# Kernel optimization log

Hardware: AMD Instinct MI355X
Metric: run time of the kernel (lower is better)

The kernel has to match this reference:

```python
import jax, jax.numpy as jnp
import numpy as np

R_MAX = 1.0
BASIS_MASK = 0xFF        # low 8 bits -> basis index (basis_size=256)
R_BITS_MASK = 0xFFFF     # next 16 bits -> quantized radius
R_DENOM = 65535.0
INT8_DENOM = 127.0


def setup_inputs() -> dict:
    key = jax.random.key(0)
    k_x, k_c, k_b, k_r, k_s, k_bias = jax.random.split(key, 6)
    B, S, D_in, D_out, BASIS = 4, 2048, 4096, 4096, 256
    x = jax.random.normal(k_x, (B, S, D_in), dtype=jnp.float32)
    codes = jax.random.randint(k_c, (D_out,), 0, 16777216, dtype=jnp.int32)
    basis_table = jax.random.normal(k_b, (BASIS, D_in), dtype=jnp.float32)
    residual_q = jax.random.randint(k_r, (D_out, D_in), 0, 256, dtype=jnp.int32)
    residual_scales = jax.random.uniform(k_s, (D_out,), dtype=jnp.float32) * 0.05
    bias = jax.random.normal(k_bias, (D_out,), dtype=jnp.float32)
    return {"x": x, "codes": codes, "basis_table": basis_table,
            "residual_q": residual_q, "residual_scales": residual_scales,
            "bias": bias}


def decode_weight(codes, basis_table, residual_q, residual_scales):
    # Bitfield decode: low 8 bits = basis index, next 16 bits = quantized radius in [0, r_max].
    idx = codes & BASIS_MASK                                   # [O]
    r = ((codes >> 8) & R_BITS_MASK).astype(jnp.float32) / R_DENOM * R_MAX  # [O]
    base = r[:, None] * basis_table[idx]                       # [O, I]
    resid = (residual_q.astype(jnp.float32) - 128.0) / INT8_DENOM  # dequant int8 residual
    return base + residual_scales[:, None] * resid             # [O, I]


def reference(x, codes, basis_table, residual_q, residual_scales, bias):
    W = decode_weight(codes, basis_table, residual_q, residual_scales)  # [O, I]
    # y = x @ W^T + bias  (fused dequant-matmul in the original CUDA kernel)
    return jnp.einsum("bsi,oi->bso", x, W) + bias
```

## Files before the change

### kernel.cpp

```cpp
#include <hip/hip_runtime.h>


typedef __bf16 bf16x8 __attribute__((ext_vector_type(8)));
typedef float f32x4 __attribute__((ext_vector_type(4)));
typedef unsigned short u16x8 __attribute__((ext_vector_type(8)));

__device__ __forceinline__ unsigned short f2bf(float f) {
    union { float f; unsigned int u; } c; c.f = f;
    unsigned int u = c.u;
    u += 0x7fffu + ((u >> 16) & 1u);
    return (unsigned short)(u >> 16);
}

__device__ __forceinline__ void load_lds16(const void* g, void* l) {
    __builtin_amdgcn_global_load_lds(
        (__attribute__((address_space(1))) void*)(void*)g,
        (__attribute__((address_space(3))) void*)l,
        16, 0, 0);
}

__global__ void decode_w_kernel(const int* __restrict__ codes,
                                const float* __restrict__ basis,
                                const int* __restrict__ q,
                                const float* __restrict__ scales,
                                unsigned short* __restrict__ Wb, int K) {
    const int o = blockIdx.x;
    const int code = codes[o];
    const int bi = code & 0xFF;
    const float r = (float)((code >> 8) & 0xFFFF) * (1.0f / 65535.0f);
    const float s = scales[o];
    const float* brow = basis + (size_t)bi * K;
    const int*   qrow = q     + (size_t)o  * K;
    unsigned short* wrow = Wb + (size_t)o  * K;
    const float inv127 = 1.0f / 127.0f;
    for (int i = threadIdx.x * 4; i < K; i += blockDim.x * 4) {
        float4 b4 = *(const float4*)(brow + i);
        int4   q4 = *(const int4*)(qrow + i);
        ushort4 w;
        w.x = f2bf(r * b4.x + s * (float)(q4.x - 128) * inv127);
        w.y = f2bf(r * b4.y + s * (float)(q4.y - 128) * inv127);
        w.z = f2bf(r * b4.z + s * (float)(q4.z - 128) * inv127);
        w.w = f2bf(r * b4.w + s * (float)(q4.w - 128) * inv127);
        *(ushort4*)(wrow + i) = w;
    }
}

__global__ void cvt_x_kernel(const float4* __restrict__ x4,
                             ushort4* __restrict__ xb4, int n4) {
    int i = blockIdx.x * blockDim.x + threadIdx.x;
    const int stride = gridDim.x * blockDim.x;
    for (; i < n4; i += stride) {
        float4 v = x4[i];
        ushort4 o;
        o.x = f2bf(v.x); o.y = f2bf(v.y); o.z = f2bf(v.z); o.w = f2bf(v.w);
        xb4[i] = o;
    }
}

#define TILE_M 128
#define TILE_N 128
#define TILE_K 32

__global__ void gemm_bt_kernel(const unsigned short* __restrict__ Xb,
                               const unsigned short* __restrict__ Wb,
                               const float* __restrict__ bias,
                               float* __restrict__ out,
                               int M, int N, int K) {
    __shared__ __align__(16) unsigned short As[TILE_M * TILE_K];
    __shared__ __align__(16) unsigned short Bs[TILE_N * TILE_K];

    const int tid  = threadIdx.x;
    const int lane = tid & 63;
    const int wv   = tid >> 6;
    const int wrow = wv >> 1;
    const int wcol = wv & 1;
    const int m0 = blockIdx.y * TILE_M;
    const int n0 = blockIdx.x * TILE_N;

    const int lr = lane & 15;
    const int kg = lane >> 4;

    f32x4 acc[4][4];
#pragma unroll
    for (int mi = 0; mi < 4; ++mi)
#pragma unroll
        for (int ni = 0; ni < 4; ++ni)
            acc[mi][ni] = (f32x4){0.f, 0.f, 0.f, 0.f};

    const int lin0 = tid, lin1 = tid + 256;
    const int ar0 = lin0 >> 2, ac0 = (lin0 & 3) * 8;
    const int ar1 = lin1 >> 2, ac1 = (lin1 & 3) * 8;

    const unsigned short* Ag0 = Xb + (size_t)(m0 + ar0) * K + ac0;
    const unsigned short* Ag1 = Xb + (size_t)(m0 + ar1) * K + ac1;
    const unsigned short* Bg0 = Wb + (size_t)(n0 + ar0) * K + ac0;
    const unsigned short* Bg1 = Wb + (size_t)(n0 + ar1) * K + ac1;

    unsigned short* Al0 = As + lin0 * 8;
    unsigned short* Al1 = As + lin1 * 8;
    unsigned short* Bl0 = Bs + lin0 * 8;
    unsigned short* Bl1 = Bs + lin1 * 8;

    for (int k0 = 0; k0 < K; k0 += TILE_K) {
        load_lds16(Ag0 + k0, Al0);
        load_lds16(Ag1 + k0, Al1);
        load_lds16(Bg0 + k0, Bl0);
        load_lds16(Bg1 + k0, Bl1);
        __syncthreads();

        bf16x8 af[4], bfr[4];
#pragma unroll
        for (int mi = 0; mi < 4; ++mi) {
            u16x8 raw = *(const u16x8*)(As + (wrow * 64 + mi * 16 + lr) * TILE_K + kg * 8);
            af[mi] = __builtin_bit_cast(bf16x8, raw);
        }
#pragma unroll
        for (int ni = 0; ni < 4; ++ni) {
            u16x8 raw = *(const u16x8*)(Bs + (wcol * 64 + ni * 16 + lr) * TILE_K + kg * 8);
            bfr[ni] = __builtin_bit_cast(bf16x8, raw);
        }
#pragma unroll
        for (int mi = 0; mi < 4; ++mi)
#pragma unroll
            for (int ni = 0; ni < 4; ++ni)
                acc[mi][ni] = __builtin_amdgcn_mfma_f32_16x16x32_bf16(
                    af[mi], bfr[ni], acc[mi][ni], 0, 0, 0);
        __syncthreads();
    }

#pragma unroll
    for (int ni = 0; ni < 4; ++ni) {
        const int n = n0 + wcol * 64 + ni * 16 + lr;
        const float bv = bias[n];
#pragma unroll
        for (int mi = 0; mi < 4; ++mi) {
            const int mbase = m0 + wrow * 64 + mi * 16 + kg * 4;
#pragma unroll
            for (int rg = 0; rg < 4; ++rg)
                out[(size_t)(mbase + rg) * N + n] = acc[mi][ni][rg] + bv;
        }
    }
}

extern "C" void kernel_launch(void* const* d_in, const int* in_sizes, int n_in,
                              void* d_out, int out_size, void* d_ws, size_t ws_size,
                              hipStream_t stream) {
    const float* x        = (const float*)d_in[0];
    const int*   codes    = (const int*)d_in[1];
    const float* basis    = (const float*)d_in[2];
    const int*   q        = (const int*)d_in[3];
    const float* scales   = (const float*)d_in[4];
    const float* bias     = (const float*)d_in[5];
    float* out = (float*)d_out;

    const int BASIS = 256;
    const int K = in_sizes[2] / BASIS;
    const int N = in_sizes[1];
    const int M = in_sizes[0] / K;

    unsigned short* Xb = (unsigned short*)d_ws;
    unsigned short* Wb = Xb + (size_t)M * K;

    const int n4 = (M * K) / 4;
    cvt_x_kernel<<<4096, 256, 0, stream>>>((const float4*)x, (ushort4*)Xb, n4);

    decode_w_kernel<<<N, 256, 0, stream>>>(codes, basis, q, scales, Wb, K);

    dim3 grid(N / TILE_N, M / TILE_M);
    gemm_bt_kernel<<<grid, 256, 0, stream>>>(Xb, Wb, bias, out, M, N, K);
}
```

Measured before the change: 568.9 us.

## Split weight into basis projection plus int8 residual GEMM with quantized activations

Rewrites y = x·W^T as r·(x·basis^T)[c] plus a residual term. The basis term becomes a small M×256 bf16 GEMM; the residual term becomes an int8 MFMA GEMM over per-row quantized activations and packed int8 residuals. The scales, gathered basis product and bias are applied in the epilogue. This removes materializing the dequantized weight and doubles MFMA throughput per instruction, at the cost of int8 activation quantization error and an extra gather from P in the epilogue.

```diff
diff --git a/kernel.cpp b/kernel.cpp
--- a/kernel.cpp
+++ b/kernel.cpp
@@ -3,14 +3,8 @@
 
 typedef __bf16 bf16x8 __attribute__((ext_vector_type(8)));
 typedef float f32x4 __attribute__((ext_vector_type(4)));
+typedef int i32x4 __attribute__((ext_vector_type(4)));
 typedef unsigned short u16x8 __attribute__((ext_vector_type(8)));
-
-__device__ __forceinline__ unsigned short f2bf(float f) {
-    union { float f; unsigned int u; } c; c.f = f;
-    unsigned int u = c.u;
-    u += 0x7fffu + ((u >> 16) & 1u);
-    return (unsigned short)(u >> 16);
-}
 
 __device__ __forceinline__ void load_lds16(const void* g, void* l) {
     __builtin_amdgcn_global_load_lds(
@@ -19,125 +13,236 @@
         16, 0, 0);
 }
 
-__global__ void decode_w_kernel(const int* __restrict__ codes,
-                                const float* __restrict__ basis,
-                                const int* __restrict__ q,
-                                const float* __restrict__ scales,
-                                unsigned short* __restrict__ Wb, int K) {
-    const int o = blockIdx.x;
-    const int code = codes[o];
-    const int bi = code & 0xFF;
-    const float r = (float)((code >> 8) & 0xFFFF) * (1.0f / 65535.0f);
-    const float s = scales[o];
-    const float* brow = basis + (size_t)bi * K;
-    const int*   qrow = q     + (size_t)o  * K;
-    unsigned short* wrow = Wb + (size_t)o  * K;
-    const float inv127 = 1.0f / 127.0f;
-    for (int i = threadIdx.x * 4; i < K; i += blockDim.x * 4) {
-        float4 b4 = *(const float4*)(brow + i);
-        int4   q4 = *(const int4*)(qrow + i);
-        ushort4 w;
-        w.x = f2bf(r * b4.x + s * (float)(q4.x - 128) * inv127);
-        w.y = f2bf(r * b4.y + s * (float)(q4.y - 128) * inv127);
-        w.z = f2bf(r * b4.z + s * (float)(q4.z - 128) * inv127);
-        w.w = f2bf(r * b4.w + s * (float)(q4.w - 128) * inv127);
-        *(ushort4*)(wrow + i) = w;
-    }
-}
-
-__global__ void cvt_x_kernel(const float4* __restrict__ x4,
-                             ushort4* __restrict__ xb4, int n4) {
-    int i = blockIdx.x * blockDim.x + threadIdx.x;
-    const int stride = gridDim.x * blockDim.x;
-    for (; i < n4; i += stride) {
-        float4 v = x4[i];
-        ushort4 o;
-        o.x = f2bf(v.x); o.y = f2bf(v.y); o.z = f2bf(v.z); o.w = f2bf(v.w);
-        xb4[i] = o;
-    }
-}
-
-#define TILE_M 128
-#define TILE_N 128
-#define TILE_K 32
-
-__global__ void gemm_bt_kernel(const unsigned short* __restrict__ Xb,
-                               const unsigned short* __restrict__ Wb,
+__global__ void quant_x_kernel(const float* __restrict__ x,
+                               signed char* __restrict__ xq,
+                               float* __restrict__ arow, int K) {
+    const int m = blockIdx.x;
+    const float* row = x + (size_t)m * K;
+    const int base = threadIdx.x * 16;
+    float4 v[4];
+#pragma unroll
+    for (int j = 0; j < 4; ++j) v[j] = *(const float4*)(row + base + j * 4);
+
+    float lmax = 0.f;
+#pragma unroll
+    for (int j = 0; j < 4; ++j) {
+        lmax = fmaxf(lmax, fabsf(v[j].x));
+        lmax = fmaxf(lmax, fabsf(v[j].y));
+        lmax = fmaxf(lmax, fabsf(v[j].z));
+        lmax = fmaxf(lmax, fabsf(v[j].w));
+    }
+#pragma unroll
+    for (int off = 32; off; off >>= 1)
+        lmax = fmaxf(lmax, __shfl_xor(lmax, off));
+    __shared__ float smax[4];
+    if ((threadIdx.x & 63) == 0) smax[threadIdx.x >> 6] = lmax;
+    __syncthreads();
+    const float mx = fmaxf(fmaxf(smax[0], smax[1]), fmaxf(smax[2], smax[3]));
+    const float inv = mx > 0.f ? 127.0f / mx : 0.0f;
+    if (threadIdx.x == 0) arow[m] = mx * (1.0f / 127.0f);
+
+    union { signed char c[16]; i32x4 w; } pk;
+#pragma unroll
+    for (int j = 0; j < 4; ++j) {
+        pk.c[j * 4 + 0] = (signed char)(int)rintf(v[j].x * inv);
+        pk.c[j * 4 + 1] = (signed char)(int)rintf(v[j].y * inv);
+        pk.c[j * 4 + 2] = (signed char)(int)rintf(v[j].z * inv);
+        pk.c[j * 4 + 3] = (signed char)(int)rintf(v[j].w * inv);
+    }
+    *(i32x4*)(xq + (size_t)m * K + base) = pk.w;
+}
+
+__global__ void pack_q_kernel(const int4* __restrict__ q4,
+                              unsigned int* __restrict__ out, int n4) {
+    const int i = blockIdx.x * blockDim.x + threadIdx.x;
+    if (i >= n4) return;
+    int4 a = q4[i];
+    unsigned int w = ((unsigned)(a.x - 128) & 0xFFu)
+                   | (((unsigned)(a.y - 128) & 0xFFu) << 8)
+                   | (((unsigned)(a.z - 128) & 0xFFu) << 16)
+                   | (((unsigned)(a.w - 128) & 0xFFu) << 24);
+    out[i] = w;
+}
+
+__global__ void p_gemm_kernel(const float* __restrict__ x,
+                              const float* __restrict__ basis,
+                              float* __restrict__ P,
+                              int M, int K) {
+    const int NB = 256;
+    __shared__ __align__(16) unsigned short As[64 * 32];
+    __shared__ __align__(16) unsigned short Bs[128 * 32];
+
+    const int tid  = threadIdx.x;
+    const int lane = tid & 63;
+    const int wv   = tid >> 6;
+    const int m0 = blockIdx.y * 64;
+    const int n0 = blockIdx.x * 128;
+    const int lr = lane & 15;
+    const int kg = lane >> 4;
+
+    f32x4 acc[4][2];
+#pragma unroll
+    for (int mi = 0; mi < 4; ++mi)
+#pragma unroll
+        for (int ni = 0; ni < 2; ++ni)
+            acc[mi][ni] = (f32x4){0.f, 0.f, 0.f, 0.f};
+
+    const int arow_ = tid >> 2, acol = (tid & 3) * 8;
+    const int lb0 = tid, lb1 = tid + 256;
+    const int br0 = lb0 >> 2, bc0 = (lb0 & 3) * 8;
+    const int br1 = lb1 >> 2, bc1 = (lb1 & 3) * 8;
+
+    const float* Agp = x + (size_t)(m0 + arow_) * K + acol;
+    const float* Bg0 = basis + (size_t)(n0 + br0) * K + bc0;
+    const float* Bg1 = basis + (size_t)(n0 + br1) * K + bc1;
+
+    for (int k0 = 0; k0 < K; k0 += 32) {
+        float4 a0 = *(const float4*)(Agp + k0);
+        float4 a1 = *(const float4*)(Agp + k0 + 4);
+        float4 b00 = *(const float4*)(Bg0 + k0);
+        float4 b01 = *(const float4*)(Bg0 + k0 + 4);
+        float4 b10 = *(const float4*)(Bg1 + k0);
+        float4 b11 = *(const float4*)(Bg1 + k0 + 4);
+        union { bf16x8 b; u16x8 u; } ca, cb0, cb1;
+        ca.b[0] = (__bf16)a0.x; ca.b[1] = (__bf16)a0.y;
+        ca.b[2] = (__bf16)a0.z; ca.b[3] = (__bf16)a0.w;
+        ca.b[4] = (__bf16)a1.x; ca.b[5] = (__bf16)a1.y;
+        ca.b[6] = (__bf16)a1.z; ca.b[7] = (__bf16)a1.w;
+        cb0.b[0] = (__bf16)b00.x; cb0.b[1] = (__bf16)b00.y;
+        cb0.b[2] = (__bf16)b00.z; cb0.b[3] = (__bf16)b00.w;
+        cb0.b[4] = (__bf16)b01.x; cb0.b[5] = (__bf16)b01.y;
+        cb0.b[6] = (__bf16)b01.z; cb0.b[7] = (__bf16)b01.w;
+        cb1.b[0] = (__bf16)b10.x; cb1.b[1] = (__bf16)b10.y;
+        cb1.b[2] = (__bf16)b10.z; cb1.b[3] = (__bf16)b10.w;
+        cb1.b[4] = (__bf16)b11.x; cb1.b[5] = (__bf16)b11.y;
+        cb1.b[6] = (__bf16)b11.z; cb1.b[7] = (__bf16)b11.w;
+        *(u16x8*)(As + tid * 8) = ca.u;
+        *(u16x8*)(Bs + lb0 * 8) = cb0.u;
+        *(u16x8*)(Bs + lb1 * 8) = cb1.u;
+        __syncthreads();
+
+        bf16x8 af[4], bfr[2];
+#pragma unroll
+        for (int mi = 0; mi < 4; ++mi)
+            af[mi] = __builtin_bit_cast(bf16x8,
+                *(const u16x8*)(As + (mi * 16 + lr) * 32 + kg * 8));
+#pragma unroll
+        for (int ni = 0; ni < 2; ++ni)
+            bfr[ni] = __builtin_bit_cast(bf16x8,
+                *(const u16x8*)(Bs + (wv * 32 + ni * 16 + lr) * 32 + kg * 8));
+#pragma unroll
+        for (int mi = 0; mi < 4; ++mi)
+#pragma unroll
+            for (int ni = 0; ni < 2; ++ni)
+                acc[mi][ni] = __builtin_amdgcn_mfma_f32_16x16x32_bf16(
+                    af[mi], bfr[ni], acc[mi][ni], 0, 0, 0);
+        __syncthreads();
+    }
+
+#pragma unroll
+    for (int ni = 0; ni < 2; ++ni) {
+        const int n = n0 + wv * 32 + ni * 16 + lr;
+#pragma unroll
+        for (int mi = 0; mi < 4; ++mi) {
+            const int mbase = m0 + mi * 16 + kg * 4;
+#pragma unroll
+            for (int rg = 0; rg < 4; ++rg)
+                P[(size_t)(mbase + rg) * NB + n] = acc[mi][ni][rg];
+        }
+    }
+}
+
+__global__ void gemm_i8_kernel(const signed char* __restrict__ Xq,
+                               const signed char* __restrict__ Qb,
+                               const float* __restrict__ arow,
+                               const int* __restrict__ codes,
+                               const float* __restrict__ scales,
                                const float* __restrict__ bias,
+                               const float* __restrict__ P,
                                float* __restrict__ out,
                                int M, int N, int K) {
-    __shared__ __align__(16) unsigned short As[TILE_M * TILE_K];
-    __shared__ __align__(16) unsigned short Bs[TILE_N * TILE_K];
+    __shared__ __align__(16) signed char As[128 * 64];
+    __shared__ __align__(16) signed char Bs[128 * 64];
 
     const int tid  = threadIdx.x;
     const int lane = tid & 63;
     const int wv   = tid >> 6;
     const int wrow = wv >> 1;
     const int wcol = wv & 1;
-    const int m0 = blockIdx.y * TILE_M;
-    const int n0 = blockIdx.x * TILE_N;
-
+    const int m0 = blockIdx.y * 128;
+    const int n0 = blockIdx.x * 128;
     const int lr = lane & 15;
     const int kg = lane >> 4;
 
-    f32x4 acc[4][4];
+    i32x4 acc[4][4];
 #pragma unroll
     for (int mi = 0; mi < 4; ++mi)
 #pragma unroll
         for (int ni = 0; ni < 4; ++ni)
-            acc[mi][ni] = (f32x4){0.f, 0.f, 0.f, 0.f};
+            acc[mi][ni] = (i32x4){0, 0, 0, 0};
 
     const int lin0 = tid, lin1 = tid + 256;
-    const int ar0 = lin0 >> 2, ac0 = (lin0 & 3) * 8;
-    const int ar1 = lin1 >> 2, ac1 = (lin1 & 3) * 8;
-
-    const unsigned short* Ag0 = Xb + (size_t)(m0 + ar0) * K + ac0;
-    const unsigned short* Ag1 = Xb + (size_t)(m0 + ar1) * K + ac1;
-    const unsigned short* Bg0 = Wb + (size_t)(n0 + ar0) * K + ac0;
-    const unsigned short* Bg1 = Wb + (size_t)(n0 + ar1) * K + ac1;
-
-    unsigned short* Al0 = As + lin0 * 8;
-    unsigned short* Al1 = As + lin1 * 8;
-    unsigned short* Bl0 = Bs + lin0 * 8;
-    unsigned short* Bl1 = Bs + lin1 * 8;
-
-    for (int k0 = 0; k0 < K; k0 += TILE_K) {
+    const int ar0 = lin0 >> 2, ac0 = (lin0 & 3) * 16;
+    const int ar1 = lin1 >> 2, ac1 = (lin1 & 3) * 16;
+
+    const signed char* Ag0 = Xq + (size_t)(m0 + ar0) * K + ac0;
+    const signed char* Ag1 = Xq + (size_t)(m0 + ar1) * K + ac1;
+    const signed char* Bg0 = Qb + (size_t)(n0 + ar0) * K + ac0;
+    const signed char* Bg1 = Qb + (size_t)(n0 + ar1) * K + ac1;
+
+    signed char* Al0 = As + lin0 * 16;
+    signed char* Al1 = As + lin1 * 16;
+    signed char* Bl0 = Bs + lin0 * 16;
+    signed char* Bl1 = Bs + lin1 * 16;
+
+    for (int k0 = 0; k0 < K; k0 += 64) {
         load_lds16(Ag0 + k0, Al0);
         load_lds16(Ag1 + k0, Al1);
         load_lds16(Bg0 + k0, Bl0);
         load_lds16(Bg1 + k0, Bl1);
         __syncthreads();
 
-        bf16x8 af[4], bfr[4];
-#pragma unroll
-        for (int mi = 0; mi < 4; ++mi) {
-            u16x8 raw = *(const u16x8*)(As + (wrow * 64 + mi * 16 + lr) * TILE_K + kg * 8);
-            af[mi] = __builtin_bit_cast(bf16x8, raw);
-        }
-#pragma unroll
-        for (int ni = 0; ni < 4; ++ni) {
-            u16x8 raw = *(const u16x8*)(Bs + (wcol * 64 + ni * 16 + lr) * TILE_K + kg * 8);
-            bfr[ni] = __builtin_bit_cast(bf16x8, raw);
-        }
+        i32x4 af[4], bfr[4];
+#pragma unroll
+        for (int mi = 0; mi < 4; ++mi)
+            af[mi] = *(const i32x4*)(As + (wrow * 64 + mi * 16 + lr) * 64 + kg * 16);
+#pragma unroll
+        for (int ni = 0; ni < 4; ++ni)
+            bfr[ni] = *(const i32x4*)(Bs + (wcol * 64 + ni * 16 + lr) * 64 + kg * 16);
 #pragma unroll
         for (int mi = 0; mi < 4; ++mi)
 #pragma unroll
             for (int ni = 0; ni < 4; ++ni)
-                acc[mi][ni] = __builtin_amdgcn_mfma_f32_16x16x32_bf16(
+                acc[mi][ni] = __builtin_amdgcn_mfma_i32_16x16x64_i8(
                     af[mi], bfr[ni], acc[mi][ni], 0, 0, 0);
         __syncthreads();
     }
+
+    float av[4][4];
+#pragma unroll
+    for (int mi = 0; mi < 4; ++mi)
+#pragma unroll
+        for (int rg = 0; rg < 4; ++rg)
+            av[mi][rg] = arow[m0 + wrow * 64 + mi * 16 + kg * 4 + rg];
 
 #pragma unroll
     for (int ni = 0; ni < 4; ++ni) {
         const int n = n0 + wcol * 64 + ni * 16 + lr;
+        const int code = codes[n];
+        const int c = code & 0xFF;
+        const float r = (float)((code >> 8) & 0xFFFF) * (1.0f / 65535.0f);
+        const float so = scales[n] * (1.0f / 127.0f);
         const float bv = bias[n];
 #pragma unroll
         for (int mi = 0; mi < 4; ++mi) {
             const int mbase = m0 + wrow * 64 + mi * 16 + kg * 4;
 #pragma unroll
-            for (int rg = 0; rg < 4; ++rg)
-                out[(size_t)(mbase + rg) * N + n] = acc[mi][ni][rg] + bv;
+            for (int rg = 0; rg < 4; ++rg) {
+                const int m = mbase + rg;
+                const float y = av[mi][rg] * so * (float)acc[mi][ni][rg]
+                              + r * P[(size_t)m * 256 + c] + bv;
+                out[(size_t)m * N + n] = y;
+            }
         }
     }
 }
@@ -158,14 +263,19 @@
     const int N = in_sizes[1];
     const int M = in_sizes[0] / K;
 
-    unsigned short* Xb = (unsigned short*)d_ws;
-    unsigned short* Wb = Xb + (size_t)M * K;
-
-    const int n4 = (M * K) / 4;
-    cvt_x_kernel<<<4096, 256, 0, stream>>>((const float4*)x, (ushort4*)Xb, n4);
-
-    decode_w_kernel<<<N, 256, 0, stream>>>(codes, basis, q, scales, Wb, K);
-
-    dim3 grid(N / TILE_N, M / TILE_M);
-    gemm_bt_kernel<<<grid, 256, 0, stream>>>(Xb, Wb, bias, out, M, N, K);
-}
+    char* ws = (char*)d_ws;
+    signed char* Xq = (signed char*)ws;
+    size_t off = (size_t)M * K;
+    float* Arow = (float*)(ws + off);
+    off += (size_t)M * sizeof(float);
+    signed char* Qb = (signed char*)(ws + off);
+    off += (size_t)N * K;
+    float* P = (float*)(ws + off);
+
+    quant_x_kernel<<<M, 256, 0, stream>>>(x, Xq, Arow, K);
+    pack_q_kernel<<<(N * K / 4 + 255) / 256, 256, 0, stream>>>(
+        (const int4*)q, (unsigned int*)Qb, N * K / 4);
+    p_gemm_kernel<<<dim3(BASIS / 128, M / 64), 256, 0, stream>>>(x, basis, P, M, K);
+    gemm_i8_kernel<<<dim3(N / 128, M / 128), 256, 0, stream>>>(
+        Xq, Qb, Arow, codes, scales, bias, P, out, M, N, K);
+}
```

New measurement: 725.5 us. +27.5%, slower.
